# Kernel optimization log

Measured on AMD Instinct MI355X. Metric: run time of the kernel, lower is better.

## Reference

```python
import jax, jax.numpy as jnp
import numpy as np

NEG_SLOPE = 0.2
EPS = 1e-16
HEADS1, OUT1 = 4, 32
HEADS2, OUT2 = 1, 32


def _gat_conv(x, W, a_src, a_dst, bias, src, dst, num_nodes, heads, out_c, concat):
    # x: [N, F_in], W: [F_in, heads*out_c], a_*: [heads, out_c]
    h = (x @ W).reshape(num_nodes, heads, out_c)            # [N, H, C]
    alpha_src = (h * a_src).sum(-1)                          # [N, H]
    alpha_dst = (h * a_dst).sum(-1)                          # [N, H]
    e = jax.nn.leaky_relu(alpha_src[src] + alpha_dst[dst], NEG_SLOPE)  # [E, H]
    # softmax over incoming edges of each destination node (PyG softmax)
    m = jax.ops.segment_max(e, dst, num_segments=num_nodes)
    ex = jnp.exp(e - m[dst])
    s = jax.ops.segment_sum(ex, dst, num_segments=num_nodes)
    alpha = ex / (s[dst] + EPS)                              # [E, H]
    out = jax.ops.segment_sum(h[src] * alpha[:, :, None], dst,
                              num_segments=num_nodes)        # [N, H, C]
    out = out.reshape(num_nodes, heads * out_c) if concat else out.mean(axis=1)
    return out + bias


def setup_inputs() -> dict:
    key = jax.random.key(0)
    ks = jax.random.split(key, 10)
    N, E, F_IN = 50000, 1600000, 128
    sc = 0.1
    return {
        "x": jax.random.normal(ks[0], (N, F_IN), jnp.float32),
        "edge_index": jax.random.randint(ks[1], (2, E), 0, N, jnp.int32),
        "W1": jax.random.normal(ks[2], (F_IN, HEADS1 * OUT1), jnp.float32) * sc,
        "a_src1": jax.random.normal(ks[3], (HEADS1, OUT1), jnp.float32) * sc,
        "a_dst1": jax.random.normal(ks[4], (HEADS1, OUT1), jnp.float32) * sc,
        "b1": jax.random.normal(ks[5], (HEADS1 * OUT1,), jnp.float32) * sc,
        "W2": jax.random.normal(ks[6], (HEADS1 * OUT1, HEADS2 * OUT2), jnp.float32) * sc,
        "a_src2": jax.random.normal(ks[7], (HEADS2, OUT2), jnp.float32) * sc,
        "a_dst2": jax.random.normal(ks[8], (HEADS2, OUT2), jnp.float32) * sc,
        "b2": jax.random.normal(ks[9], (OUT2,), jnp.float32) * sc,
    }


def reference(x, edge_index, W1, a_src1, a_dst1, b1, W2, a_src2, a_dst2, b2):
    N = x.shape[0]
    # PyG GATConv default add_self_loops=True
    loops = jnp.arange(N, dtype=edge_index.dtype)
    src = jnp.concatenate([edge_index[0], loops])
    dst = jnp.concatenate([edge_index[1], loops])
    h = _gat_conv(x, W1, a_src1, a_dst1, b1, src, dst, N, HEADS1, OUT1, True)
    h = jax.nn.elu(h)
    return _gat_conv(h, W2, a_src2, a_dst2, b2, src, dst, N, HEADS2, OUT2, False)
```

## Files before the change

kernel.cpp:

```cpp
#include <hip/hip_runtime.h>
#include <math.h>

#define NEG_SLOPE 0.2f
#define EPSV 1e-16f
#define NPART 8

typedef _Float16 half4 __attribute__((ext_vector_type(4)));
typedef _Float16 half8 __attribute__((ext_vector_type(8)));
typedef float floatx2 __attribute__((ext_vector_type(2)));


__global__ void k_scan_blk(const int* __restrict__ degp, int N,
                           int* __restrict__ rowptr, int* __restrict__ bsum){
    int b = blockIdx.x, t = threadIdx.x;
    int base = b * 1024 + t * 4;
    int v[4];
    #pragma unroll
    for (int j = 0; j < 4; j++){
        int n = base + j, s = 0;
        if (n < N){
            #pragma unroll
            for (int p = 0; p < NPART; p++) s += degp[p * N + n];
        }
        v[j] = s;
    }
    int s = v[0] + v[1] + v[2] + v[3];
    int lane = t & 63, wid = t >> 6;
    int x = s;
    #pragma unroll
    for (int off = 1; off < 64; off <<= 1){
        int y = __shfl_up(x, off, 64);
        if (lane >= off) x += y;
    }
    __shared__ int ws[4];
    if (lane == 63) ws[wid] = x;
    __syncthreads();
    int woff = 0;
    for (int w = 0; w < wid; w++) woff += ws[w];
    int run = woff + x - s;
    #pragma unroll
    for (int j = 0; j < 4; j++){
        if (base + j < N) rowptr[base + j] = run;
        run += v[j];
    }
    if (t == 255) bsum[b] = woff + x;
}

__global__ void k_finalize(const int* __restrict__ bsum, const int* __restrict__ degp,
                           int N, int ET,
                           int* __restrict__ rowptr, int* __restrict__ poff){
    int b = blockIdx.x, t = threadIdx.x;
    int n = b * 256 + t;
    int chunk = (b * 256) >> 10;
    int off = 0;
    for (int c = 0; c < chunk; c++) off += bsum[c];
    if (n < N){
        int r = rowptr[n] + off;
        rowptr[n] = r;
        int run = r;
        #pragma unroll
        for (int p = 0; p < NPART; p++){
            poff[p * N + n] = run;
            run += degp[p * N + n];
        }
    }
    if (n == 0) rowptr[N] = ET;
}

__launch_bounds__(256)
__global__ void k_scatter2(const int* __restrict__ ei, int E, int ET, int N,
                           const int* __restrict__ poff,
                           const unsigned short* __restrict__ rank,
                           int* __restrict__ csr_src){
    int i = blockIdx.x * 256 + threadIdx.x;
    if (i >= ET) return;
    int s, d;
    if (i < E){ s = ei[i]; d = ei[E + i]; } else { s = i - E; d = s; }
    int pr = rank[i];
    int p = pr >> 13, r = pr & 0x1FFF;
    csr_src[poff[p * N + d] + r] = s;
}


__launch_bounds__(256, 5)
__global__ void k_gemm1_hist(const float* __restrict__ x, const float* __restrict__ W1,
                             const float* __restrict__ a_src, const float* __restrict__ a_dst,
                             _Float16* __restrict__ h1h, float* __restrict__ asrc1,
                             float* __restrict__ adst1, int N, int nGemmBlk,
                             const int* __restrict__ ei, int E, int ET,
                             unsigned int* __restrict__ degp, unsigned short* __restrict__ rank){
    __shared__ float xl[64 * 128];
    int t = threadIdx.x;
    if ((int)blockIdx.x >= nGemmBlk){
        int p = __builtin_amdgcn_s_getreg((3 << 11) | 20) & 7;
        int base = (blockIdx.x - nGemmBlk) * 1024 + t;
        #pragma unroll
        for (int j = 0; j < 4; j++){
            int i = base + j * 256;
            if (i < ET){
                int d = (i < E) ? ei[E + i] : (i - E);
                unsigned r = __hip_atomic_fetch_add(&degp[(size_t)p * N + d], 1u,
                                 __ATOMIC_RELAXED, __HIP_MEMORY_SCOPE_WORKGROUP);
                rank[i] = (unsigned short)((p << 13) | r);
            }
        }
        return;
    }
    int cg = t & 31, rs = t >> 5;
    int n0 = blockIdx.x * 64;
    for (int idx = t; idx < 2048; idx += 256){
        int row = idx >> 5, k4 = idx & 31;
        float4 v = {0.f, 0.f, 0.f, 0.f};
        if (n0 + row < N) v = *(const float4*)&x[(size_t)(n0 + row) * 128 + k4 * 4];
        *(float4*)&xl[row * 128 + k4 * 4] = v;
    }
    __syncthreads();
    float4 acc[8];
    #pragma unroll
    for (int j = 0; j < 8; j++) acc[j] = (float4){0.f, 0.f, 0.f, 0.f};
    for (int hc = 0; hc < 16; hc++){
        float4 wr[8];
        #pragma unroll
        for (int k = 0; k < 8; k++)
            wr[k] = *(const float4*)&W1[(hc * 8 + k) * 128 + cg * 4];
        #pragma unroll
        for (int kb = 0; kb < 8; kb += 4){
            float4 xv[8];
            #pragma unroll
            for (int j = 0; j < 8; j++)
                xv[j] = *(const float4*)&xl[(rs + 8 * j) * 128 + hc * 8 + kb];
            #pragma unroll
            for (int kk = 0; kk < 4; kk++){
                float4 w = wr[kb + kk];
                #pragma unroll
                for (int j = 0; j < 8; j++){
                    float xs = ((const float*)&xv[j])[kk];
                    acc[j].x = fmaf(xs, w.x, acc[j].x);
                    acc[j].y = fmaf(xs, w.y, acc[j].y);
                    acc[j].z = fmaf(xs, w.z, acc[j].z);
                    acc[j].w = fmaf(xs, w.w, acc[j].w);
                }
            }
        }
    }
    float4 a4s = *(const float4*)&a_src[cg * 4];
    float4 a4d = *(const float4*)&a_dst[cg * 4];
    #pragma unroll
    for (int j = 0; j < 8; j++){
        int n = n0 + rs + 8 * j;
        if (n >= N) continue;
        float4 a = acc[j];
        half4 hv;
        hv.x = (_Float16)a.x; hv.y = (_Float16)a.y;
        hv.z = (_Float16)a.z; hv.w = (_Float16)a.w;
        *(half4*)&h1h[((size_t)n << 7) + (cg << 2)] = hv;
        float vs = a.x * a4s.x + a.y * a4s.y + a.z * a4s.z + a.w * a4s.w;
        float vd = a.x * a4d.x + a.y * a4d.y + a.z * a4d.z + a.w * a4d.w;
        #pragma unroll
        for (int m = 1; m <= 4; m <<= 1){
            vs += __shfl_xor(vs, m, 64);
            vd += __shfl_xor(vd, m, 64);
        }
        if ((cg & 7) == 0){
            int head = cg >> 3;
            asrc1[n * 4 + head] = vs;
            adst1[n * 4 + head] = vd;
        }
    }
}


__launch_bounds__(256)
__global__ void k_agg1(const int* __restrict__ rowptr, const int* __restrict__ csr_src,
                       const float* __restrict__ asrc1, const float* __restrict__ adst1,
                       const _Float16* __restrict__ h1h,
                       const float* __restrict__ b1, float* __restrict__ x2, int N){
    int t = threadIdx.x;
    int lane = t & 63;
    int g = lane >> 4, l = lane & 15, head = l >> 2;
    int n = blockIdx.x * 16 + ((t >> 6) << 2) + g;
    bool valid = (n < N);
    int nn = valid ? n : 0;
    int start = rowptr[nn], end = rowptr[nn + 1];
    float adn = adst1[(nn << 2) + head];
    const char* hb = (const char*)h1h;
    const char* ab = (const char*)asrc1;
    int hoff = l << 4;
    int aoff = head << 2;
    floatx2 r0[4], r1[4], r2[4], r3[4];
    #pragma unroll
    for (int j = 0; j < 4; j++){
        r0[j] = (floatx2)0.f; r1[j] = (floatx2)0.f;
        r2[j] = (floatx2)0.f; r3[j] = (floatx2)0.f;
    }
    float s0a = 0.f, s1a = 0.f, s2a = 0.f, s3a = 0.f;
    int i = start;
    for (; i + 3 < end; i += 4){
        int sa = csr_src[i];
        int sb = csr_src[i + 1];
        int sc = csr_src[i + 2];
        int sd = csr_src[i + 3];
        float ea = *(const float*)(ab + (sa << 4) + aoff) + adn;
        float eb = *(const float*)(ab + (sb << 4) + aoff) + adn;
        float ec = *(const float*)(ab + (sc << 4) + aoff) + adn;
        float ed = *(const float*)(ab + (sd << 4) + aoff) + adn;
        ea = fmaxf(ea, NEG_SLOPE * ea);
        eb = fmaxf(eb, NEG_SLOPE * eb);
        ec = fmaxf(ec, NEG_SLOPE * ec);
        ed = fmaxf(ed, NEG_SLOPE * ed);
        float wa = __expf(ea);
        float wb = __expf(eb);
        float wc = __expf(ec);
        float wd = __expf(ed);
        half8 ha = *(const half8*)(hb + (sa << 8) + hoff);
        half8 hbv = *(const half8*)(hb + (sb << 8) + hoff);
        half8 hcv = *(const half8*)(hb + (sc << 8) + hoff);
        half8 hdv = *(const half8*)(hb + (sd << 8) + hoff);
        s0a += wa; s1a += wb; s2a += wc; s3a += wd;
        floatx2 wa2 = {wa, wa}, wb2 = {wb, wb}, wc2 = {wc, wc}, wd2 = {wd, wd};
        #pragma unroll
        for (int j = 0; j < 4; j++){
            floatx2 ca = {(float)ha[2*j], (float)ha[2*j+1]};
            floatx2 cb = {(float)hbv[2*j], (float)hbv[2*j+1]};
            floatx2 cc = {(float)hcv[2*j], (float)hcv[2*j+1]};
            floatx2 cd = {(float)hdv[2*j], (float)hdv[2*j+1]};
            r0[j] = wa2 * ca + r0[j];
            r1[j] = wb2 * cb + r1[j];
            r2[j] = wc2 * cc + r2[j];
            r3[j] = wd2 * cd + r3[j];
        }
    }
    for (; i < end; i++){
        int sa = csr_src[i];
        float ea = *(const float*)(ab + (sa << 4) + aoff) + adn;
        ea = fmaxf(ea, NEG_SLOPE * ea);
        float wa = __expf(ea);
        half8 ha = *(const half8*)(hb + (sa << 8) + hoff);
        s0a += wa;
        floatx2 wa2 = {wa, wa};
        #pragma unroll
        for (int j = 0; j < 4; j++){
            floatx2 ca = {(float)ha[2*j], (float)ha[2*j+1]};
            r0[j] = wa2 * ca + r0[j];
        }
    }
    if (valid){
        float ssum = (s0a + s1a) + (s2a + s3a);
        float inv = 1.f / (ssum + EPSV);
        float o[8];
        #pragma unroll
        for (int j = 0; j < 4; j++){
            floatx2 c = (r0[j] + r1[j]) + (r2[j] + r3[j]);
            float v0 = c.x * inv + b1[l * 8 + 2*j];
            float v1 = c.y * inv + b1[l * 8 + 2*j + 1];
            o[2*j]   = (v0 > 0.f) ? v0 : expm1f(v0);
            o[2*j+1] = (v1 > 0.f) ? v1 : expm1f(v1);
        }
        float4 o0 = {o[0], o[1], o[2], o[3]};
        float4 o1 = {o[4], o[5], o[6], o[7]};
        *(float4*)&x2[((size_t)n << 7) + (l << 3)]     = o0;
        *(float4*)&x2[((size_t)n << 7) + (l << 3) + 4] = o1;
    }
}


__launch_bounds__(256)
__global__ void k_gemm2(const float* __restrict__ x2, const float* __restrict__ W2,
                        const float* __restrict__ a_src, const float* __restrict__ a_dst,
                        _Float16* __restrict__ h2h, float* __restrict__ asrc2,
                        float* __restrict__ adst2, int N){
    __shared__ float Wl[128 * 32];
    __shared__ float xl[64 * 128];
    int t = threadIdx.x;
    int cg = t & 7, ns = t >> 3;
    for (int idx = t; idx < 1024; idx += 256)
        *(float4*)&Wl[idx * 4] = *(const float4*)&W2[idx * 4];
    int n0 = blockIdx.x * 64;
    for (int idx = t; idx < 2048; idx += 256){
        int row = idx >> 5, k4 = idx & 31;
        float4 v = {0.f, 0.f, 0.f, 0.f};
        if (n0 + row < N) v = *(const float4*)&x2[(size_t)(n0 + row) * 128 + k4 * 4];
        *(float4*)&xl[row * 128 + k4 * 4] = v;
    }
    __syncthreads();
    float4 acc0 = {0,0,0,0}, acc1 = {0,0,0,0};
    #pragma unroll 2
    for (int k = 0; k < 128; k += 4){
        float4 xv0 = *(float4*)&xl[(ns      ) * 128 + k];
        float4 xv1 = *(float4*)&xl[(ns + 32) * 128 + k];
        #pragma unroll
        for (int kk = 0; kk < 4; kk++){
            float4 w = *(float4*)&Wl[(k + kk) * 32 + cg * 4];
            float x0 = ((float*)&xv0)[kk];
            float x1 = ((float*)&xv1)[kk];
            acc0.x = fmaf(x0, w.x, acc0.x); acc0.y = fmaf(x0, w.y, acc0.y);
            acc0.z = fmaf(x0, w.z, acc0.z); acc0.w = fmaf(x0, w.w, acc0.w);
            acc1.x = fmaf(x1, w.x, acc1.x); acc1.y = fmaf(x1, w.y, acc1.y);
            acc1.z = fmaf(x1, w.z, acc1.z); acc1.w = fmaf(x1, w.w, acc1.w);
        }
    }
    float4 a4s = *(const float4*)&a_src[cg * 4];
    float4 a4d = *(const float4*)&a_dst[cg * 4];
    float4 accs[2] = {acc0, acc1};
    #pragma unroll
    for (int j = 0; j < 2; j++){
        int n = n0 + ns + 32 * j;
        if (n >= N) continue;
        float4 a = accs[j];
        half4 hv;
        hv.x = (_Float16)a.x; hv.y = (_Float16)a.y;
        hv.z = (_Float16)a.z; hv.w = (_Float16)a.w;
        *(half4*)&h2h[((size_t)n << 5) + (cg << 2)] = hv;
        float vs = a.x * a4s.x + a.y * a4s.y + a.z * a4s.z + a.w * a4s.w;
        float vd = a.x * a4d.x + a.y * a4d.y + a.z * a4d.z + a.w * a4d.w;
        #pragma unroll
        for (int m = 1; m <= 4; m <<= 1){
            vs += __shfl_xor(vs, m, 64);
            vd += __shfl_xor(vd, m, 64);
        }
        if (cg == 0){ asrc2[n] = vs; adst2[n] = vd; }
    }
}


__launch_bounds__(256)
__global__ void k_agg2(const int* __restrict__ rowptr, const int* __restrict__ csr_src,
                       const float* __restrict__ asrc2, const float* __restrict__ adst2,
                       const _Float16* __restrict__ h2h,
                       const float* __restrict__ b2, float* __restrict__ out, int N){
    int t = threadIdx.x;
    int lane = t & 63;
    int g = lane >> 3, l = lane & 7;
    int n = blockIdx.x * 32 + ((t >> 6) << 3) + g;
    bool valid = (n < N);
    int nn = valid ? n : 0;
    int start = rowptr[nn], end = rowptr[nn + 1];
    float adn = adst2[nn];
    const char* hb = (const char*)h2h;
    const char* ab = (const char*)asrc2;
    int hoff = l << 3;
    floatx2 a0[2], a1[2], a2[2], a3[2];
    a0[0] = (floatx2)0.f; a0[1] = (floatx2)0.f;
    a1[0] = (floatx2)0.f; a1[1] = (floatx2)0.f;
    a2[0] = (floatx2)0.f; a2[1] = (floatx2)0.f;
    a3[0] = (floatx2)0.f; a3[1] = (floatx2)0.f;
    float s0a = 0.f, s1a = 0.f, s2a = 0.f, s3a = 0.f;
    int i = start;
    for (; i + 3 < end; i += 4){
        int sa = csr_src[i];
        int sb = csr_src[i + 1];
        int sc = csr_src[i + 2];
        int sd = csr_src[i + 3];
        float ea = *(const float*)(ab + (sa << 2)) + adn;
        float eb = *(const float*)(ab + (sb << 2)) + adn;
        float ec = *(const float*)(ab + (sc << 2)) + adn;
        float ed = *(const float*)(ab + (sd << 2)) + adn;
        ea = fmaxf(ea, NEG_SLOPE * ea);
        eb = fmaxf(eb, NEG_SLOPE * eb);
        ec = fmaxf(ec, NEG_SLOPE * ec);
        ed = fmaxf(ed, NEG_SLOPE * ed);
        float wa = __expf(ea);
        float wb = __expf(eb);
        float wc = __expf(ec);
        float wd = __expf(ed);
        half4 ha = *(const half4*)(hb + (sa << 6) + hoff);
        half4 hbv = *(const half4*)(hb + (sb << 6) + hoff);
        half4 hcv = *(const half4*)(hb + (sc << 6) + hoff);
        half4 hdv = *(const half4*)(hb + (sd << 6) + hoff);
        s0a += wa; s1a += wb; s2a += wc; s3a += wd;
        floatx2 wa2 = {wa, wa}, wb2 = {wb, wb}, wc2 = {wc, wc}, wd2 = {wd, wd};
        floatx2 ca0 = {(float)ha.x, (float)ha.y},  ca1 = {(float)ha.z, (float)ha.w};
        floatx2 cb0 = {(float)hbv.x, (float)hbv.y}, cb1 = {(float)hbv.z, (float)hbv.w};
        floatx2 cc0 = {(float)hcv.x, (float)hcv.y}, cc1 = {(float)hcv.z, (float)hcv.w};
        floatx2 cd0 = {(float)hdv.x, (float)hdv.y}, cd1 = {(float)hdv.z, (float)hdv.w};
        a0[0] = wa2 * ca0 + a0[0]; a0[1] = wa2 * ca1 + a0[1];
        a1[0] = wb2 * cb0 + a1[0]; a1[1] = wb2 * cb1 + a1[1];
        a2[0] = wc2 * cc0 + a2[0]; a2[1] = wc2 * cc1 + a2[1];
        a3[0] = wd2 * cd0 + a3[0]; a3[1] = wd2 * cd1 + a3[1];
    }
    for (; i < end; i++){
        int sa = csr_src[i];
        float ea = *(const float*)(ab + (sa << 2)) + adn;
        ea = fmaxf(ea, NEG_SLOPE * ea);
        float wa = __expf(ea);
        half4 ha = *(const half4*)(hb + (sa << 6) + hoff);
        s0a += wa;
        floatx2 wa2 = {wa, wa};
        floatx2 ca0 = {(float)ha.x, (float)ha.y}, ca1 = {(float)ha.z, (float)ha.w};
        a0[0] = wa2 * ca0 + a0[0]; a0[1] = wa2 * ca1 + a0[1];
    }
    if (valid){
        floatx2 m0 = (a0[0] + a1[0]) + (a2[0] + a3[0]);
        floatx2 m1 = (a0[1] + a1[1]) + (a2[1] + a3[1]);
        float ssum = (s0a + s1a) + (s2a + s3a);
        float inv = 1.f / (ssum + EPSV);
        const float4 b4 = *(const float4*)&b2[l * 4];
        float4 o;
        o.x = m0.x * inv + b4.x; o.y = m0.y * inv + b4.y;
        o.z = m1.x * inv + b4.z; o.w = m1.y * inv + b4.w;
        *(float4*)&out[((size_t)n << 5) + (l << 2)] = o;
    }
}


extern "C" void kernel_launch(void* const* d_in, const int* in_sizes, int n_in,
                              void* d_out, int out_size, void* d_ws, size_t ws_size,
                              hipStream_t stream){
    const float* x      = (const float*)d_in[0];
    const int*   ei     = (const int*)  d_in[1];
    const float* W1     = (const float*)d_in[2];
    const float* a_src1 = (const float*)d_in[3];
    const float* a_dst1 = (const float*)d_in[4];
    const float* b1     = (const float*)d_in[5];
    const float* W2     = (const float*)d_in[6];
    const float* a_src2 = (const float*)d_in[7];
    const float* a_dst2 = (const float*)d_in[8];
    const float* b2     = (const float*)d_in[9];
    float* out = (float*)d_out;

    int N  = in_sizes[0] / 128;
    int E  = in_sizes[1] / 2;
    int ET = E + N;
    int nScanBlk = (N + 1023) / 1024;
    int G  = (ET + 255) / 256;
    int GH = (ET + 1023) / 1024;
    int nGemmBlk = (N + 63) / 64;

    char* ws = (char*)d_ws;
    size_t off = 0;
    auto alloc = [&](size_t bytes) -> char* {
        char* p = ws + off;
        off += (bytes + 255) & ~(size_t)255;
        return p;
    };
    int*            degp    = (int*)           alloc((size_t)NPART * N * 4);
    int*            rowptr  = (int*)           alloc((size_t)(N + 1) * 4);
    int*            bsum    = (int*)           alloc((size_t)nScanBlk * 4);
    unsigned short* rank    = (unsigned short*)alloc((size_t)ET * 2);
    int*            poff    = (int*)           alloc((size_t)NPART * N * 4);
    int*            csr_src = (int*)           alloc((size_t)ET * 4);
    _Float16*       h1h     = (_Float16*)      alloc((size_t)N * 128 * 2);
    float*          x2      = (float*)         alloc((size_t)N * 128 * 4);
    float*          asrc1   = (float*)         alloc((size_t)N * 4 * 4);
    float*          adst1   = (float*)         alloc((size_t)N * 4 * 4);
    _Float16*       h2h     = (_Float16*)      alloc((size_t)N * 32 * 2);
    float*          asrc2   = (float*)         alloc((size_t)N * 4);
    float*          adst2   = (float*)         alloc((size_t)N * 4);

    hipMemsetAsync(degp, 0, (size_t)NPART * N * 4, stream);
    hipLaunchKernelGGL(k_gemm1_hist, dim3(nGemmBlk + GH), dim3(256), 0, stream,
                       x, W1, a_src1, a_dst1, h1h, asrc1, adst1, N, nGemmBlk,
                       ei, E, ET, (unsigned int*)degp, rank);
    hipLaunchKernelGGL(k_scan_blk,  dim3(nScanBlk), dim3(256), 0, stream, degp, N, rowptr, bsum);
    hipLaunchKernelGGL(k_finalize,  dim3((N + 255) / 256), dim3(256), 0, stream, bsum, degp, N, ET, rowptr, poff);
    hipLaunchKernelGGL(k_scatter2,  dim3(G), dim3(256), 0, stream, ei, E, ET, N, poff, rank, csr_src);
    hipLaunchKernelGGL(k_agg1,      dim3((N + 15) / 16), dim3(256), 0, stream, rowptr, csr_src, asrc1, adst1, h1h, b1, x2, N);
    hipLaunchKernelGGL(k_gemm2,     dim3((N + 63) / 64), dim3(256), 0, stream, x2, W2, a_src2, a_dst2, h2h, asrc2, adst2, N);
    hipLaunchKernelGGL(k_agg2,      dim3((N + 31) / 32), dim3(256), 0, stream, rowptr, csr_src, asrc2, adst2, h2h, b2, out, N);
}
```

Before: 301.9 us.

## Use fp16 MFMA for layer-1 GEMM with folded attention projection

```diff
diff --git a/kernel.cpp b/kernel.cpp
--- a/kernel.cpp
+++ b/kernel.cpp
@@ -8,6 +8,7 @@
 typedef _Float16 half4 __attribute__((ext_vector_type(4)));
 typedef _Float16 half8 __attribute__((ext_vector_type(8)));
 typedef float floatx2 __attribute__((ext_vector_type(2)));
+typedef float f32x4 __attribute__((ext_vector_type(4)));
 
 
 __global__ void k_scan_blk(const int* __restrict__ degp, int N,
@@ -82,14 +83,53 @@
 }
 
 
-__launch_bounds__(256, 5)
-__global__ void k_gemm1_hist(const float* __restrict__ x, const float* __restrict__ W1,
-                             const float* __restrict__ a_src, const float* __restrict__ a_dst,
+__global__ void k_pack(const float* __restrict__ W1, const float* __restrict__ a_src,
+                       const float* __restrict__ a_dst,
+                       _Float16* __restrict__ W1f, _Float16* __restrict__ Uf){
+    int b = blockIdx.x, t = threadIdx.x;
+    if (b < 32){
+        #pragma unroll
+        for (int i = 0; i < 2; i++){
+            int idx = t + 256 * i;
+            int jj = idx & 7, ln = idx >> 3;
+            int kt = b & 3, ct = b >> 2;
+            int k = kt * 32 + (ln >> 4) * 8 + jj;
+            int col = ct * 16 + (ln & 15);
+            W1f[b * 512 + idx] = (_Float16)W1[k * 128 + col];
+        }
+        return;
+    }
+    __shared__ float U[128 * 8];
+    if (t < 128){
+        #pragma unroll
+        for (int h = 0; h < 4; h++){
+            float s = 0.f, d = 0.f;
+            for (int cc = 0; cc < 32; cc++){
+                float w = W1[t * 128 + h * 32 + cc];
+                s += w * a_src[h * 32 + cc];
+                d += w * a_dst[h * 32 + cc];
+            }
+            U[t * 8 + h]     = s;
+            U[t * 8 + h + 4] = d;
+        }
+    }
+    __syncthreads();
+    for (int idx = t; idx < 4 * 64 * 8; idx += 256){
+        int jj = idx & 7, ln = (idx >> 3) & 63, kt = idx >> 9;
+        int k = kt * 32 + (ln >> 4) * 8 + jj;
+        int col = ln & 15;
+        Uf[idx] = (_Float16)(col < 8 ? U[k * 8 + col] : 0.f);
+    }
+}
+
+
+__launch_bounds__(256, 4)
+__global__ void k_gemm1_hist(const float* __restrict__ x, const _Float16* __restrict__ W1f,
+                             const _Float16* __restrict__ Uf,
                              _Float16* __restrict__ h1h, float* __restrict__ asrc1,
                              float* __restrict__ adst1, int N, int nGemmBlk,
                              const int* __restrict__ ei, int E, int ET,
                              unsigned int* __restrict__ degp, unsigned short* __restrict__ rank){
-    __shared__ float xl[64 * 128];
     int t = threadIdx.x;
     if ((int)blockIdx.x >= nGemmBlk){
         int p = __builtin_amdgcn_s_getreg((3 << 11) | 20) & 7;
@@ -106,66 +146,56 @@
         }
         return;
     }
-    int cg = t & 31, rs = t >> 5;
-    int n0 = blockIdx.x * 64;
-    for (int idx = t; idx < 2048; idx += 256){
-        int row = idx >> 5, k4 = idx & 31;
-        float4 v = {0.f, 0.f, 0.f, 0.f};
-        if (n0 + row < N) v = *(const float4*)&x[(size_t)(n0 + row) * 128 + k4 * 4];
-        *(float4*)&xl[row * 128 + k4 * 4] = v;
-    }
-    __syncthreads();
-    float4 acc[8];
-    #pragma unroll
-    for (int j = 0; j < 8; j++) acc[j] = (float4){0.f, 0.f, 0.f, 0.f};
-    for (int hc = 0; hc < 16; hc++){
-        float4 wr[8];
-        #pragma unroll
-        for (int k = 0; k < 8; k++)
-            wr[k] = *(const float4*)&W1[(hc * 8 + k) * 128 + cg * 4];
-        #pragma unroll
-        for (int kb = 0; kb < 8; kb += 4){
-            float4 xv[8];
-            #pragma unroll
-            for (int j = 0; j < 8; j++)
-                xv[j] = *(const float4*)&xl[(rs + 8 * j) * 128 + hc * 8 + kb];
-            #pragma unroll
-            for (int kk = 0; kk < 4; kk++){
-                float4 w = wr[kb + kk];
-                #pragma unroll
-                for (int j = 0; j < 8; j++){
-                    float xs = ((const float*)&xv[j])[kk];
-                    acc[j].x = fmaf(xs, w.x, acc[j].x);
-                    acc[j].y = fmaf(xs, w.y, acc[j].y);
-                    acc[j].z = fmaf(xs, w.z, acc[j].z);
-                    acc[j].w = fmaf(xs, w.w, acc[j].w);
-                }
-            }
-        }
-    }
-    float4 a4s = *(const float4*)&a_src[cg * 4];
-    float4 a4d = *(const float4*)&a_dst[cg * 4];
-    #pragma unroll
-    for (int j = 0; j < 8; j++){
-        int n = n0 + rs + 8 * j;
+    int w = t >> 6, lane = t & 63;
+    int arow = blockIdx.x * 64 + w * 16 + (lane & 15);
+    bool arow_ok = (arow < N);
+    const float4* xr = (const float4*)&x[(size_t)(arow_ok ? arow : 0) << 7];
+    const half8* Wf = (const half8*)W1f;
+    const half8* Uv = (const half8*)Uf;
+
+    f32x4 acc[8];
+    #pragma unroll
+    for (int c = 0; c < 8; c++) acc[c] = (f32x4)0.f;
+    f32x4 accA = (f32x4)0.f;
+
+    #pragma unroll
+    for (int kt = 0; kt < 4; kt++){
+        half8 af;
+        if (arow_ok){
+            float4 p0 = xr[kt * 8 + (lane >> 4) * 2];
+            float4 p1 = xr[kt * 8 + (lane >> 4) * 2 + 1];
+            af[0] = (_Float16)p0.x; af[1] = (_Float16)p0.y;
+            af[2] = (_Float16)p0.z; af[3] = (_Float16)p0.w;
+            af[4] = (_Float16)p1.x; af[5] = (_Float16)p1.y;
+            af[6] = (_Float16)p1.z; af[7] = (_Float16)p1.w;
+        } else {
+            af[0] = (_Float16)0.f; af[1] = (_Float16)0.f;
+            af[2] = (_Float16)0.f; af[3] = (_Float16)0.f;
+            af[4] = (_Float16)0.f; af[5] = (_Float16)0.f;
+            af[6] = (_Float16)0.f; af[7] = (_Float16)0.f;
+        }
+        #pragma unroll
+        for (int ct = 0; ct < 8; ct++){
+            half8 bf = Wf[(ct * 4 + kt) * 64 + lane];
+            acc[ct] = __builtin_amdgcn_mfma_f32_16x16x32_f16(af, bf, acc[ct], 0, 0, 0);
+        }
+        half8 uf = Uv[kt * 64 + lane];
+        accA = __builtin_amdgcn_mfma_f32_16x16x32_f16(af, uf, accA, 0, 0, 0);
+    }
+
+    int g = lane >> 4, j = lane & 15;
+    int rowbase = blockIdx.x * 64 + w * 16 + g * 4;
+    #pragma unroll
+    for (int r = 0; r < 4; r++){
+        int n = rowbase + r;
         if (n >= N) continue;
-        float4 a = acc[j];
-        half4 hv;
-        hv.x = (_Float16)a.x; hv.y = (_Float16)a.y;
-        hv.z = (_Float16)a.z; hv.w = (_Float16)a.w;
-        *(half4*)&h1h[((size_t)n << 7) + (cg << 2)] = hv;
-        float vs = a.x * a4s.x + a.y * a4s.y + a.z * a4s.z + a.w * a4s.w;
-        float vd = a.x * a4d.x + a.y * a4d.y + a.z * a4d.z + a.w * a4d.w;
-        #pragma unroll
-        for (int m = 1; m <= 4; m <<= 1){
-            vs += __shfl_xor(vs, m, 64);
-            vd += __shfl_xor(vd, m, 64);
-        }
-        if ((cg & 7) == 0){
-            int head = cg >> 3;
-            asrc1[n * 4 + head] = vs;
-            adst1[n * 4 + head] = vd;
-        }
+        _Float16* hrow = &h1h[(size_t)n << 7];
+        #pragma unroll
+        for (int ct = 0; ct < 8; ct++)
+            hrow[ct * 16 + j] = (_Float16)acc[ct][r];
+        float av = accA[r];
+        if (j < 4)            asrc1[n * 4 + j]       = av;
+        else if (j < 8)       adst1[n * 4 + (j - 4)] = av;
     }
 }
 
@@ -446,10 +476,13 @@
     _Float16*       h2h     = (_Float16*)      alloc((size_t)N * 32 * 2);
     float*          asrc2   = (float*)         alloc((size_t)N * 4);
     float*          adst2   = (float*)         alloc((size_t)N * 4);
+    _Float16*       W1f     = (_Float16*)      alloc((size_t)32 * 512 * 2);
+    _Float16*       Uf      = (_Float16*)      alloc((size_t)4 * 512 * 2);
 
     hipMemsetAsync(degp, 0, (size_t)NPART * N * 4, stream);
+    hipLaunchKernelGGL(k_pack, dim3(33), dim3(256), 0, stream, W1, a_src1, a_dst1, W1f, Uf);
     hipLaunchKernelGGL(k_gemm1_hist, dim3(nGemmBlk + GH), dim3(256), 0, stream,
-                       x, W1, a_src1, a_dst1, h1h, asrc1, adst1, N, nGemmBlk,
+                       x, W1f, Uf, h1h, asrc1, adst1, N, nGemmBlk,
                        ei, E, ET, (unsigned int*)degp, rank);
     hipLaunchKernelGGL(k_scan_blk,  dim3(nScanBlk), dim3(256), 0, stream, degp, N, rowptr, bsum);
     hipLaunchKernelGGL(k_finalize,  dim3((N + 255) / 256), dim3(256), 0, stream, bsum, degp, N, ET, rowptr, poff);
```

Result: no change. 303.7 us (+0.6%).
